# Kernel optimization log

Hardware: AMD Instinct MI355X
Metric: run time of the kernel (lower is better)

Reference implementation:

```python
import math
import jax, jax.numpy as jnp
import numpy as np

B, T, D, K, R, KC = 4, 2048, 1024, 8, 16, 4
H = 4 * D  # mlp hidden


def setup_inputs() -> dict:
    key = jax.random.key(0)
    ks = jax.random.split(key, 12)
    s = lambda i, shape: jax.random.normal(ks[i], shape, jnp.float32) * 0.02
    # state_decay_logit init: geometric decays in [dmin, dmax], logit = log(p) - log1p(-p)
    dmin, dmax = 0.9, 0.999
    dec = np.exp(np.linspace(math.log(dmin), math.log(dmax), K))
    decay_logit = jnp.asarray(np.log(dec) - np.log1p(-dec), jnp.float32)
    return dict(
        x=jax.random.normal(ks[0], (B, T, D), jnp.float32),
        conv_w=s(1, (D, 1, KC)),            # depthwise conv kernel (torch Conv1d weight)
        gp_w=s(2, (D, D)), gp_b=jnp.zeros((D,), jnp.float32),
        up_w=s(3, (D, H)), up_b=jnp.zeros((H,), jnp.float32),
        dn_w=s(4, (H, D)), dn_b=jnp.zeros((D,), jnp.float32),
        si_w=s(5, (D, K * D)),              # state_in (no bias)
        so_w=s(6, (K * D, D)),              # state_out (no bias)
        decay_logit=decay_logit,
        rs_w=s(7, (D, R)), rs_b=jnp.zeros((R,), jnp.float32),
        rwg_w=s(8, (D, 1)), rwg_b=jnp.zeros((1,), jnp.float32),
        rv_w=s(9, (D, D)), rv_b=jnp.zeros((D,), jnp.float32),
        gr_w=s(10, (D, 1)), gr_b=jnp.zeros((1,), jnp.float32),
        gl_w=s(11, (D, 1)), gl_b=jnp.zeros((1,), jnp.float32),
    )


def _rms_norm(x, eps=1e-6):
    return x * jax.lax.rsqrt(jnp.mean(x * x, axis=-1, keepdims=True) + eps)


def _forward(x, conv_w, gp_w, gp_b, up_w, up_b, dn_w, dn_b, si_w, so_w,
             decay_logit, rs_w, rs_b, rwg_w, rwg_b, rv_w, rv_b, gr_w, gr_b, gl_w, gl_b):
    Bx, Tx, Dx = x.shape
    u = _rms_norm(x)
    # --- local mixer: causal depthwise conv + sigmoid gate + SiLU MLP ---
    xc = jax.lax.conv_general_dilated(
        jnp.swapaxes(u, 1, 2), conv_w, window_strides=(1,),
        padding=[(KC - 1, 0)], feature_group_count=Dx,
        dimension_numbers=('NCH', 'OIH', 'NCH'))
    xc = jnp.swapaxes(xc, 1, 2)                       # (B,T,D) causal conv output
    xg = xc * jax.nn.sigmoid(xc @ gp_w + gp_b)
    local = jax.nn.silu(xg @ up_w + up_b) @ dn_w + dn_b
    # --- per-channel exponential-decay state + register read/write scan ---
    dec = jax.nn.sigmoid(decay_logit)                 # (K,)
    z = (u @ si_w).reshape(Bx, Tx, K, Dx)             # state_in, (B,T,K,D)
    sel = jax.nn.softmax(u @ rs_w + rs_b, axis=-1)    # soft register address (B,T,R)
    wg = jax.nn.sigmoid(u @ rwg_w + rwg_b)            # write gate (B,T,1)
    v = u @ rv_w + rv_b                                # register value (B,T,D)

    def step(carry, inp):
        s, regs = carry
        z_t, sel_t, w_t, v_t = inp
        read = jnp.einsum('br,brd->bd', sel_t, regs)  # soft read before write
        ws = (w_t * sel_t)[:, :, None]                # (B,R,1)
        regs = regs * (1.0 - ws) + ws * v_t[:, None, :]
        s = dec[None, :, None] * s + z_t
        return (s, regs), (s, read)

    init = (jnp.zeros((Bx, K, Dx), x.dtype), jnp.zeros((Bx, R, Dx), x.dtype))
    tm = lambda a: jnp.swapaxes(a, 0, 1)              # time-major for scan
    _, (s_all, reads) = jax.lax.scan(step, init, (tm(z), tm(sel), tm(wg), tm(v)))
    s_all = tm(s_all)                                 # (B,T,K,D)
    reads = tm(reads)                                 # (B,T,D)
    long_out = jnp.einsum('btkd,kde->bte', s_all, so_w.reshape(K, Dx, Dx))
    g_long = jax.nn.sigmoid(u @ gl_w + gl_b)
    g_reg = jax.nn.sigmoid(u @ gr_w + gr_b)
    return x + local + g_long * long_out + g_reg * reads


def reference(x, conv_w, gp_w, gp_b, up_w, up_b, dn_w, dn_b, si_w, so_w,
              decay_logit, rs_w, rs_b, rwg_w, rwg_b, rv_w, rv_b, gr_w, gr_b, gl_w, gl_b):
    return _forward(x, conv_w, gp_w, gp_b, up_w, up_b, dn_w, dn_b, si_w, so_w,
                    decay_logit, rs_w, rs_b, rwg_w, rwg_b, rv_w, rv_b, gr_w, gr_b, gl_w, gl_b)
```

## Files before the change

### kernel.cpp

```cpp
#include <hip/hip_runtime.h>

typedef unsigned short u16;
typedef __bf16 bf16x8 __attribute__((ext_vector_type(8)));
typedef float f32x4 __attribute__((ext_vector_type(4)));
typedef u16 u16x4 __attribute__((ext_vector_type(4)));

#define D_ 1024
#define T_ 2048
#define B_ 4
#define K_ 8
#define R_ 16
#define H_ 4096
#define NROW (B_*T_)
#define CH 32
#define CL (T_/CH)
#define CHS 64
#define CLS (T_/CHS)

__device__ __forceinline__ u16 f2bf(float f){
  union{float f;unsigned u;} v; v.f=f;
  unsigned r = v.u + 0x7FFFu + ((v.u>>16)&1u);
  return (u16)(r>>16);
}
__device__ __forceinline__ float bf2f(u16 b){
  union{unsigned u;float f;} v; v.u = ((unsigned)b)<<16; return v.f;
}
__device__ __forceinline__ float sigm(float x){ return 1.f/(1.f+__expf(-x)); }

__device__ __forceinline__ void gload_lds16(const void* g, void* l){
  __builtin_amdgcn_global_load_lds((const __attribute__((address_space(1))) void*)g,
                                   (__attribute__((address_space(3))) void*)l, 16, 0, 0);
}

__global__ __launch_bounds__(256) void fill_k(float* __restrict__ out, long n, float v){
  long i = (long)blockIdx.x*256 + threadIdx.x;
  if (i < n) out[i] = v;
}

__global__ __launch_bounds__(256) void transpose_cast(const float* __restrict__ in, u16* __restrict__ out,
                                                      int R, int C){
  __shared__ float tile[32][33];
  int bx = blockIdx.x*32;
  int by = blockIdx.y*32;
  int tx = threadIdx.x & 31, ty = threadIdx.x >> 5;
  #pragma unroll
  for (int i=0;i<32;i+=8) tile[ty+i][tx] = in[(size_t)(by+ty+i)*C + bx+tx];
  __syncthreads();
  #pragma unroll
  for (int i=0;i<32;i+=8) out[(size_t)(bx+ty+i)*R + by+tx] = f2bf(tile[tx][ty+i]);
}

__global__ __launch_bounds__(256) void castbf(const float* __restrict__ in, u16* __restrict__ out, long n){
  long i = (long)blockIdx.x*256 + threadIdx.x;
  if (i < n) out[i] = f2bf(in[i]);
}

__global__ __launch_bounds__(256) void initout_k(const float* __restrict__ x, const float* __restrict__ b,
                                                 float* __restrict__ out){
  size_t i = ((size_t)blockIdx.x*256 + threadIdx.x)*4;
  f32x4 xv = *(const f32x4*)(x + i);
  f32x4 bv = *(const f32x4*)(b + (i & (D_-1)));
  xv += bv;
  *(f32x4*)(out + i) = xv;
}

__global__ __launch_bounds__(256) void rmsnorm_k(const float* __restrict__ x, u16* __restrict__ u){
  int row = blockIdx.x;
  const float* xr = x + (size_t)row*D_;
  float xv[4]; float ss = 0.f;
  #pragma unroll
  for (int i=0;i<4;i++){ xv[i] = xr[threadIdx.x + 256*i]; ss += xv[i]*xv[i]; }
  #pragma unroll
  for (int o=32;o>0;o>>=1) ss += __shfl_down(ss, o);
  __shared__ float red[4];
  if ((threadIdx.x&63)==0) red[threadIdx.x>>6] = ss;
  __syncthreads();
  float tot = red[0]+red[1]+red[2]+red[3];
  float r = rsqrtf(tot*(1.f/D_) + 1e-6f);
  #pragma unroll
  for (int i=0;i<4;i++) u[(size_t)row*D_ + threadIdx.x + 256*i] = f2bf(xv[i]*r);
}

__global__ __launch_bounds__(256) void conv_k(const u16* __restrict__ u, const float* __restrict__ w,
                                              u16* __restrict__ xc){
  size_t base = ((size_t)blockIdx.x*256 + threadIdx.x)*4;
  int t  = (int)((base >> 10) & (T_-1));
  int d0 = (int)(base & (D_-1));
  f32x4 wv[4];
  #pragma unroll
  for (int jj=0;jj<4;jj++) wv[jj] = *(const f32x4*)&w[(d0+jj)*4];
  float acc[4] = {0.f,0.f,0.f,0.f};
  #pragma unroll
  for (int j=0;j<4;j++){
    if (t-3+j >= 0){
      u16x4 uv = *(const u16x4*)(u + base + (long)(j-3)*D_);
      #pragma unroll
      for (int jj=0;jj<4;jj++) acc[jj] += bf2f(uv[jj]) * wv[jj][j];
    }
  }
  u16x4 o;
  #pragma unroll
  for (int jj=0;jj<4;jj++) o[jj] = f2bf(acc[jj]);
  *(u16x4*)(xc + base) = o;
}

__global__ __launch_bounds__(256) void smalln_k(const u16* __restrict__ u,
    const float* __restrict__ rs_w, const float* __restrict__ rs_b,
    const float* __restrict__ rwg_w, const float* __restrict__ rwg_b,
    const float* __restrict__ gl_w, const float* __restrict__ gl_b,
    const float* __restrict__ gr_w, const float* __restrict__ gr_b,
    float* __restrict__ sel, float* __restrict__ wg, float* __restrict__ gl, float* __restrict__ gr){
  int row = blockIdx.x, tid = threadIdx.x;
  float p[19];
  #pragma unroll
  for (int c=0;c<19;c++) p[c] = 0.f;
  for (int i=0;i<4;i++){
    int e = tid + i*256;
    float ue = bf2f(u[(size_t)row*D_ + e]);
    const float* rw = rs_w + (size_t)e*16;
    #pragma unroll
    for (int r=0;r<16;r++) p[r] += ue*rw[r];
    p[16] += ue*rwg_w[e];
    p[17] += ue*gl_w[e];
    p[18] += ue*gr_w[e];
  }
  __shared__ float red[19*4];
  #pragma unroll
  for (int c=0;c<19;c++){
    float v = p[c];
    #pragma unroll
    for (int o=32;o>0;o>>=1) v += __shfl_down(v, o);
    if ((tid&63)==0) red[c*4 + (tid>>6)] = v;
  }
  __syncthreads();
  if (tid==0){
    float s[19];
    #pragma unroll
    for (int c=0;c<19;c++) s[c] = red[c*4]+red[c*4+1]+red[c*4+2]+red[c*4+3];
    float mx = -1e30f;
    #pragma unroll
    for (int r=0;r<16;r++){ s[r] += rs_b[r]; mx = fmaxf(mx, s[r]); }
    float ssum = 0.f;
    #pragma unroll
    for (int r=0;r<16;r++){ s[r] = __expf(s[r]-mx); ssum += s[r]; }
    float inv = 1.f/ssum;
    #pragma unroll
    for (int r=0;r<16;r++) sel[(size_t)row*16+r] = s[r]*inv;
    wg[row] = sigm(s[16] + rwg_b[0]);
    gl[row] = sigm(s[17] + gl_b[0]);
    gr[row] = sigm(s[18] + gr_b[0]);
  }
}

#define BM 128
#define BN 128
#define BK 32

template<int EPI>
__global__ __launch_bounds__(256)
void gemm_bt(const u16* __restrict__ A, const u16* __restrict__ BT,
             void* __restrict__ outp, const float* __restrict__ bias,
             const void* __restrict__ aux,
             int K, int lda, int ldb, int ldc,
             long zA, long zB, long zC)
{
  __shared__ __attribute__((aligned(16))) u16 As[BM*BK];
  __shared__ __attribute__((aligned(16))) u16 Bs[BN*BK];
  int nwg = gridDim.x*gridDim.y;
  int bx = blockIdx.x, by = blockIdx.y;
  if ((nwg & 7) == 0){
    int bid = blockIdx.y*gridDim.x + blockIdx.x;
    int cpx = nwg >> 3;
    int s = (bid & 7)*cpx + (bid >> 3);
    bx = s % gridDim.x; by = s / gridDim.x;
  }
  const u16* Ab = A + (size_t)blockIdx.z*zA + (size_t)bx*BM*lda;
  const u16* Bb = BT + (size_t)blockIdx.z*zB + (size_t)by*BN*ldb;
  int tid = threadIdx.x, lane = tid&63, wid = tid>>6;
  int wr = wid>>1, wc = wid&1;
  f32x4 acc[4][4];
  #pragma unroll
  for (int m=0;m<4;m++)
    #pragma unroll
    for (int n=0;n<4;n++) acc[m][n] = (f32x4){0.f,0.f,0.f,0.f};

  int srow = lane>>2;
  int scol = (lane&3)*8;
  int klo  = (lane>>4)*8;
  for (int k0=0; k0<K; k0+=BK){
    #pragma unroll
    for (int i=0;i<2;i++){
      int r0 = wid*32 + i*16;
      gload_lds16(Ab + (size_t)(r0+srow)*lda + k0 + scol, &As[r0*BK]);
      gload_lds16(Bb + (size_t)(r0+srow)*ldb + k0 + scol, &Bs[r0*BK]);
    }
    __syncthreads();
    bf16x8 af[4], bfr[4];
    #pragma unroll
    for (int m=0;m<4;m++) af[m] = *(const bf16x8*)&As[(wr*64+m*16+(lane&15))*BK + klo];
    #pragma unroll
    for (int n=0;n<4;n++) bfr[n] = *(const bf16x8*)&Bs[(wc*64+n*16+(lane&15))*BK + klo];
    #pragma unroll
    for (int m=0;m<4;m++)
      #pragma unroll
      for (int n=0;n<4;n++)
        acc[m][n] = __builtin_amdgcn_mfma_f32_16x16x32_bf16(af[m], bfr[n], acc[m][n], 0, 0, 0);
    __syncthreads();
  }

  size_t obase = (size_t)blockIdx.z*zC;
  int row0 = bx*BM + wr*64;
  int col0 = by*BN + wc*64;
  #pragma unroll
  for (int m=0;m<4;m++){
    #pragma unroll
    for (int n=0;n<4;n++){
      int col = col0 + n*16 + (lane&15);
      #pragma unroll
      for (int r=0;r<4;r++){
        int row = row0 + m*16 + (lane>>4)*4 + r;
        float c = acc[m][n][r];
        size_t idx = obase + (size_t)row*ldc + col;
        if (EPI==0){ ((u16*)outp)[idx] = f2bf(c); }
        else if (EPI==1){ ((u16*)outp)[idx] = f2bf(c + bias[col]); }
        else if (EPI==2){ float t=c+bias[col]; ((u16*)outp)[idx] = f2bf(bf2f(((const u16*)aux)[idx]) * sigm(t)); }
        else if (EPI==3){ float t=c+bias[col]; ((u16*)outp)[idx] = f2bf(t*sigm(t)); }
        else if (EPI==4){ ((float*)outp)[idx] = ((const float*)aux)[idx] + c + bias[col]; }
        else            { ((float*)outp)[idx] += c; }
      }
    }
  }
}

template<int NT, int EPI>
__global__ __launch_bounds__(512, 2)
void gemm8p(const u16* __restrict__ A, const u16* __restrict__ BT,
            void* __restrict__ outp, const float* __restrict__ bias,
            const void* __restrict__ aux,
            int lda, int ldb, int ldc, long zA, long zB, long zC,
            int rx, int ry, int nry)
{
  __shared__ __attribute__((aligned(16))) u16 lds8[65536];
  int bid = blockIdx.y*gridDim.x + blockIdx.x;
  int xcd = bid & 7;
  int s   = bid >> 3;
  int rgx = xcd / nry, rgy = xcd - rgx*nry;
  int bx = rgx*rx + (s % rx);
  int by = rgy*ry + (s / rx);

  const u16* Ab = A + (size_t)blockIdx.z*zA + (size_t)bx*256*lda;
  const u16* Bb = BT + (size_t)blockIdx.z*zB + (size_t)by*256*ldb;

  int tid = threadIdx.x, l = tid&63, w = tid>>6;
  int wr = w>>2, wc = w&3;
  int rS0 = (w*2+0)*8 + (l>>3);
  int rS1 = (w*2+1)*8 + (l>>3);
  int cg  = (((l&7) ^ (l>>3)) << 3);
  int seg0 = (w*2+0)*512;
  int seg1 = (w*2+1)*512;

  auto STAGE = [&](int h){
    int kt = h>>2, idx = h&3, par = kt&1;
    int koff = kt*64;
    if (idx < 2){
      const u16* s0 = Bb + (size_t)(idx*128 + rS0)*ldb + koff + cg;
      const u16* s1 = Bb + (size_t)(idx*128 + rS1)*ldb + koff + cg;
      u16* d = &lds8[par*32768 + 16384 + idx*8192];
      gload_lds16(s0, d + seg0);
      gload_lds16(s1, d + seg1);
    } else {
      int a = idx-2;
      const u16* s0 = Ab + (size_t)(a*128 + rS0)*lda + koff + cg;
      const u16* s1 = Ab + (size_t)(a*128 + rS1)*lda + koff + cg;
      u16* d = &lds8[par*32768 + a*8192];
      gload_lds16(s0, d + seg0);
      gload_lds16(s1, d + seg1);
    }
  };

  f32x4 acc[8][4];
  #pragma unroll
  for (int m=0;m<8;m++)
    #pragma unroll
    for (int n=0;n<4;n++) acc[m][n] = (f32x4){0.f,0.f,0.f,0.f};

  for (int h=0; h<7; ++h) STAGE(h);
  asm volatile("s_waitcnt vmcnt(6)" ::: "memory");
  __builtin_amdgcn_s_barrier();

  for (int it=0; it<NT/2; ++it){
    #pragma unroll
    for (int sub=0; sub<2; ++sub){
      int kt = it*2+sub;
      const int par = sub;
      u16* Abase = &lds8[par*32768 + wr*8192];
      u16* Bbase = &lds8[par*32768 + 16384 + (wc>>1)*8192];
      bf16x8 bf[4][2];
      #pragma unroll
      for (int q=0; q<4; ++q){
        bf16x8 af[2][2];
        if (q==0){
          #pragma unroll
          for (int n=0;n<4;n++)
            #pragma unroll
            for (int ss=0;ss<2;ss++){
              int rr = (wc&1)*64 + n*16 + (l&15);
              int c16 = (l>>4) + ss*4;
              bf[n][ss] = *(const bf16x8*)&Bbase[rr*64 + ((c16 ^ (rr&7))<<3)];
            }
        }
        #pragma unroll
        for (int i=0;i<2;i++)
          #pragma unroll
          for (int ss=0;ss<2;ss++){
            int rr = q*32 + i*16 + (l&15);
            int c16 = (l>>4) + ss*4;
            af[i][ss] = *(const bf16x8*)&Abase[rr*64 + ((c16 ^ (rr&7))<<3)];
          }
        __builtin_amdgcn_sched_barrier(0);
        int h = kt*4 + q + 7;
        if (h < 4*NT) STAGE(h);
        __builtin_amdgcn_s_barrier();
        asm volatile("s_waitcnt lgkmcnt(0)" ::: "memory");
        __builtin_amdgcn_sched_barrier(0);
        __builtin_amdgcn_s_setprio(1);
        #pragma unroll
        for (int i=0;i<2;i++)
          #pragma unroll
          for (int n=0;n<4;n++)
            #pragma unroll
            for (int ss=0;ss<2;ss++)
              acc[q*2+i][n] = __builtin_amdgcn_mfma_f32_16x16x32_bf16(af[i][ss], bf[n][ss], acc[q*2+i][n], 0, 0, 0);
        __builtin_amdgcn_s_setprio(0);
        if (q==3){
          if (kt == NT-2)      asm volatile("s_waitcnt vmcnt(0)" ::: "memory");
          else if (kt < NT-2)  asm volatile("s_waitcnt vmcnt(6)" ::: "memory");
        }
        __builtin_amdgcn_s_barrier();
      }
    }
  }

  size_t obase = (size_t)blockIdx.z*zC;
  int row0 = bx*256 + wr*128;
  int col0 = by*256 + wc*64;
  #pragma unroll
  for (int m=0;m<8;m++){
    #pragma unroll
    for (int n=0;n<4;n++){
      int col = col0 + n*16 + (l&15);
      #pragma unroll
      for (int r=0;r<4;r++){
        int row = row0 + m*16 + (l>>4)*4 + r;
        float c = acc[m][n][r];
        size_t idx = obase + (size_t)row*ldc + col;
        if (EPI==0){ ((u16*)outp)[idx] = f2bf(c); }
        else if (EPI==1){ ((u16*)outp)[idx] = f2bf(c + bias[col]); }
        else if (EPI==2){ float t=c+bias[col]; ((u16*)outp)[idx] = f2bf(bf2f(((const u16*)aux)[idx]) * sigm(t)); }
        else if (EPI==3){ float t=c+bias[col]; ((u16*)outp)[idx] = f2bf(t*sigm(t)); }
        else            { unsafeAtomicAdd(&((float*)outp)[idx], c); }
      }
    }
  }
}

template<int NT>
__global__ __launch_bounds__(512, 2)
void gemm8z(const u16* __restrict__ A, const u16* __restrict__ BT,
            void* __restrict__ outp, const float* __restrict__ bias,
            const float* __restrict__ bias2, const void* __restrict__ aux,
            int lda, int ldb, int ldc, long zA, long zB, long zC,
            int rx, int ry, int nry)
{
  __shared__ __attribute__((aligned(16))) u16 lds8[65536];
  int bid = blockIdx.y*gridDim.x + blockIdx.x;
  int xcd = bid & 7;
  int s   = bid >> 3;
  int rgx = xcd / nry, rgy = xcd - rgx*nry;
  int bx = rgx*rx + (s % rx);
  int by = rgy*ry + (s / rx);

  const u16* Ab = A + (size_t)blockIdx.z*zA + (size_t)bx*256*lda;
  const u16* Bb = BT + (size_t)blockIdx.z*zB + (size_t)by*256*ldb;

  int tid = threadIdx.x, l = tid&63, w = tid>>6;
  int wr = w>>2, wc = w&3;
  int rS0 = (w*2+0)*8 + (l>>3);
  int rS1 = (w*2+1)*8 + (l>>3);
  int cg  = (((l&7) ^ (l>>3)) << 3);
  int seg0 = (w*2+0)*512;
  int seg1 = (w*2+1)*512;

  auto STAGE = [&](int h){
    int kt = h>>2, idx = h&3, par = kt&1;
    int koff = kt*64;
    if (idx < 2){
      const u16* s0 = Bb + (size_t)(idx*128 + rS0)*ldb + koff + cg;
      const u16* s1 = Bb + (size_t)(idx*128 + rS1)*ldb + koff + cg;
      u16* d = &lds8[par*32768 + 16384 + idx*8192];
      gload_lds16(s0, d + seg0);
      gload_lds16(s1, d + seg1);
    } else {
      int a = idx-2;
      const u16* s0 = Ab + (size_t)(a*128 + rS0)*lda + koff + cg;
      const u16* s1 = Ab + (size_t)(a*128 + rS1)*lda + koff + cg;
      u16* d = &lds8[par*32768 + a*8192];
      gload_lds16(s0, d + seg0);
      gload_lds16(s1, d + seg1);
    }
  };

  f32x4 acc[8][4];
  #pragma unroll
  for (int m=0;m<8;m++)
    #pragma unroll
    for (int n=0;n<4;n++) acc[m][n] = (f32x4){0.f,0.f,0.f,0.f};

  for (int h=0; h<7; ++h) STAGE(h);
  asm volatile("s_waitcnt vmcnt(6)" ::: "memory");
  __builtin_amdgcn_s_barrier();

  for (int it=0; it<NT/2; ++it){
    #pragma unroll
    for (int sub=0; sub<2; ++sub){
      int kt = it*2+sub;
      const int par = sub;
      u16* Abase = &lds8[par*32768 + wr*8192];
      u16* Bbase = &lds8[par*32768 + 16384 + (wc>>1)*8192];
      bf16x8 bf[4][2];
      #pragma unroll
      for (int q=0; q<4; ++q){
        bf16x8 af[2][2];
        if (q==0){
          #pragma unroll
          for (int n=0;n<4;n++)
            #pragma unroll
            for (int ss=0;ss<2;ss++){
              int rr = (wc&1)*64 + n*16 + (l&15);
              int c16 = (l>>4) + ss*4;
              bf[n][ss] = *(const bf16x8*)&Bbase[rr*64 + ((c16 ^ (rr&7))<<3)];
            }
        }
        #pragma unroll
        for (int i=0;i<2;i++)
          #pragma unroll
          for (int ss=0;ss<2;ss++){
            int rr = q*32 + i*16 + (l&15);
            int c16 = (l>>4) + ss*4;
            af[i][ss] = *(const bf16x8*)&Abase[rr*64 + ((c16 ^ (rr&7))<<3)];
          }
        __builtin_amdgcn_sched_barrier(0);
        int h = kt*4 + q + 7;
        if (h < 4*NT) STAGE(h);
        __builtin_amdgcn_s_barrier();
        asm volatile("s_waitcnt lgkmcnt(0)" ::: "memory");
        __builtin_amdgcn_sched_barrier(0);
        __builtin_amdgcn_s_setprio(1);
        #pragma unroll
        for (int i=0;i<2;i++)
          #pragma unroll
          for (int n=0;n<4;n++)
            #pragma unroll
            for (int ss=0;ss<2;ss++)
              acc[q*2+i][n] = __builtin_amdgcn_mfma_f32_16x16x32_bf16(af[i][ss], bf[n][ss], acc[q*2+i][n], 0, 0, 0);
        __builtin_amdgcn_s_setprio(0);
        if (q==3){
          if (kt == NT-2)      asm volatile("s_waitcnt vmcnt(0)" ::: "memory");
          else if (kt < NT-2)  asm volatile("s_waitcnt vmcnt(6)" ::: "memory");
        }
        __builtin_amdgcn_s_barrier();
      }
    }
  }

  size_t obase = (size_t)blockIdx.z*zC;
  int row0 = bx*256 + wr*128;
  int col0 = by*256 + wc*64;
  bool z0 = (blockIdx.z == 0);
  #pragma unroll
  for (int m=0;m<8;m++){
    #pragma unroll
    for (int n=0;n<4;n++){
      int col = col0 + n*16 + (l&15);
      #pragma unroll
      for (int r=0;r<4;r++){
        int row = row0 + m*16 + (l>>4)*4 + r;
        float c = acc[m][n][r];
        size_t idx = obase + (size_t)row*ldc + col;
        if (z0){ float t=c+bias[col]; ((u16*)outp)[idx] = f2bf(bf2f(((const u16*)aux)[idx]) * sigm(t)); }
        else   { ((u16*)outp)[idx] = f2bf(c + bias2[col]); }
      }
    }
  }
}

template<int NT, int EPI>
__global__ __launch_bounds__(512, 2)
void gemm2p(const u16* __restrict__ A, const u16* __restrict__ BT,
            void* __restrict__ outp, const float* __restrict__ bias,
            const void* __restrict__ aux,
            int lda, int ldb, int ldc, long zA, long zB, long zC,
            int rx, int ry, int nry)
{
  __shared__ __attribute__((aligned(16))) u16 lds8[65536];
  int bid = blockIdx.y*gridDim.x + blockIdx.x;
  int xcd = bid & 7;
  int s   = bid >> 3;
  int rgx = xcd / nry, rgy = xcd - rgx*nry;
  int bx = rgx*rx + (s % rx);
  int by = rgy*ry + (s / rx);

  const u16* Ab = A + (size_t)blockIdx.z*zA + (size_t)bx*256*lda;
  const u16* Bb = BT + (size_t)blockIdx.z*zB + (size_t)by*256*ldb;

  int tid = threadIdx.x, l = tid&63, w = tid>>6;
  int wr = w>>2, wc = w&3;
  int cg  = (((l&7) ^ (l>>3)) << 3);
  const u16* gA0 = Ab + (size_t)((w*2+0)*8 + (l>>3))*lda + cg;
  const u16* gA1 = Ab + (size_t)((w*2+1)*8 + (l>>3))*lda + cg;
  const u16* gB0 = Bb + (size_t)((w*2+0)*8 + (l>>3))*ldb + cg;
  const u16* gB1 = Bb + (size_t)((w*2+1)*8 + (l>>3))*ldb + cg;
  size_t a128 = (size_t)128*lda, b128 = (size_t)128*ldb;
  int seg0 = (w*2+0)*512, seg1 = (w*2+1)*512;

  auto STAGE_TILE = [&](int par){
    u16* Ad = &lds8[par*32768];
    u16* Bd = &lds8[par*32768 + 16384];
    gload_lds16(gB0,        Bd + seg0);
    gload_lds16(gB1,        Bd + seg1);
    gload_lds16(gB0 + b128, Bd + 8192 + seg0);
    gload_lds16(gB1 + b128, Bd + 8192 + seg1);
    gload_lds16(gA0,        Ad + seg0);
    gload_lds16(gA1,        Ad + seg1);
    gload_lds16(gA0 + a128, Ad + 8192 + seg0);
    gload_lds16(gA1 + a128, Ad + 8192 + seg1);
    gA0 += 64; gA1 += 64; gB0 += 64; gB1 += 64;
  };

  f32x4 acc[8][4];
  #pragma unroll
  for (int m=0;m<8;m++)
    #pragma unroll
    for (int n=0;n<4;n++) acc[m][n] = (f32x4){0.f,0.f,0.f,0.f};

  STAGE_TILE(0);
  asm volatile("s_waitcnt vmcnt(0)" ::: "memory");
  __builtin_amdgcn_s_barrier();
  __builtin_amdgcn_sched_barrier(0);

  for (int kt=0; kt<NT; ++kt){
    int par = kt&1;
    if (kt+1 < NT) STAGE_TILE(par^1);
    u16* Abase = &lds8[par*32768 + wr*8192];
    u16* Bbase = &lds8[par*32768 + 16384 + (wc>>1)*8192];
    bf16x8 bf[4][2];
    #pragma unroll
    for (int n=0;n<4;n++)
      #pragma unroll
      for (int ss=0;ss<2;ss++){
        int rr = (wc&1)*64 + n*16 + (l&15);
        int c16 = (l>>4) + ss*4;
        bf[n][ss] = *(const bf16x8*)&Bbase[rr*64 + ((c16 ^ (rr&7))<<3)];
      }
    __builtin_amdgcn_s_setprio(1);
    #pragma unroll
    for (int q=0;q<4;q++){
      bf16x8 af[2][2];
      #pragma unroll
      for (int i=0;i<2;i++)
        #pragma unroll
        for (int ss=0;ss<2;ss++){
          int rr = q*32 + i*16 + (l&15);
          int c16 = (l>>4) + ss*4;
          af[i][ss] = *(const bf16x8*)&Abase[rr*64 + ((c16 ^ (rr&7))<<3)];
        }
      #pragma unroll
      for (int i=0;i<2;i++)
        #pragma unroll
        for (int n=0;n<4;n++)
          #pragma unroll
          for (int ss=0;ss<2;ss++)
            acc[q*2+i][n] = __builtin_amdgcn_mfma_f32_16x16x32_bf16(af[i][ss], bf[n][ss], acc[q*2+i][n], 0, 0, 0);
    }
    __builtin_amdgcn_s_setprio(0);
    asm volatile("s_waitcnt vmcnt(0)" ::: "memory");
    __builtin_amdgcn_s_barrier();
    __builtin_amdgcn_sched_barrier(0);
  }

  size_t obase = (size_t)blockIdx.z*zC;
  int row0 = bx*256 + wr*128;
  int col0 = by*256 + wc*64;
  #pragma unroll
  for (int m=0;m<8;m++){
    #pragma unroll
    for (int n=0;n<4;n++){
      int col = col0 + n*16 + (l&15);
      #pragma unroll
      for (int r=0;r<4;r++){
        int row = row0 + m*16 + (l>>4)*4 + r;
        float c = acc[m][n][r];
        size_t idx = obase + (size_t)row*ldc + col;
        if (EPI==0){ ((u16*)outp)[idx] = f2bf(c); }
        else if (EPI==1){ ((u16*)outp)[idx] = f2bf(c + bias[col]); }
        else if (EPI==2){ float t=c+bias[col]; ((u16*)outp)[idx] = f2bf(bf2f(((const u16*)aux)[idx]) * sigm(t)); }
        else if (EPI==3){ float t=c+bias[col]; ((u16*)outp)[idx] = f2bf(t*sigm(t)); }
        else            { unsafeAtomicAdd(&((float*)outp)[idx], c); }
      }
    }
  }
}

template<int KH>
__global__ __launch_bounds__(256) void scan_s1v(const u16* __restrict__ y, const float* __restrict__ logit,
                                                int p, float* __restrict__ Hend){
  int e0 = threadIdx.x*4;
  int c = blockIdx.y, b = blockIdx.z;
  float dec[KH]; f32x4 h[KH];
  #pragma unroll
  for (int k=0;k<KH;k++){ dec[k] = sigm(logit[KH*p+k]); h[k] = (f32x4){0.f,0.f,0.f,0.f}; }
  size_t row0 = (size_t)b*T_ + (size_t)c*CLS;
  for (int t=0;t<CLS;t++){
    const u16* yp = y + (row0+t)*(size_t)(KH*D_) + e0;
    #pragma unroll
    for (int k=0;k<KH;k++){
      u16x4 w = *(const u16x4*)(yp + (size_t)k*D_);
      #pragma unroll
      for (int j=0;j<4;j++) h[k][j] = dec[k]*h[k][j] + bf2f(w[j]);
    }
  }
  #pragma unroll
  for (int k=0;k<KH;k++)
    *(f32x4*)&Hend[(((size_t)b*CHS+c)*KH+k)*D_ + e0] = h[k];
}

template<int KH>
__global__ __launch_bounds__(256) void scan_s2v(const float* __restrict__ Hend, const float* __restrict__ logit,
                                                int p, float* __restrict__ Sinit){
  int idx = blockIdx.x*256 + threadIdx.x;
  if (idx >= B_*KH*D_) return;
  int e = idx % D_; int kh = (idx/D_) % KH; int b = idx/(D_*KH);
  float dec = sigm(logit[KH*p+kh]);
  float dL = powf(dec, (float)CLS);
  float carry = 0.f;
  for (int c=0;c<CHS;c++){
    size_t i3 = (((size_t)b*CHS+c)*KH+kh)*D_ + e;
    Sinit[i3] = carry;
    carry = dL*carry + Hend[i3];
  }
}

template<int KH>
__global__ __launch_bounds__(256) void scan_s3v(const u16* __restrict__ y, const float* __restrict__ logit,
                                                int p, const float* __restrict__ Sinit,
                                                const float* __restrict__ glb, float* __restrict__ out){
  int e0 = threadIdx.x*4;
  int c = blockIdx.y, b = blockIdx.z;
  float dec[KH]; f32x4 h[KH];
  #pragma unroll
  for (int k=0;k<KH;k++){
    dec[k] = sigm(logit[KH*p+k]);
    h[k] = *(const f32x4*)&Sinit[(((size_t)b*CHS+c)*KH+k)*D_ + e0];
  }
  size_t row0 = (size_t)b*T_ + (size_t)c*CLS;
  for (int t=0;t<CLS;t++){
    const u16* yp = y + (row0+t)*(size_t)(KH*D_) + e0;
    f32x4 sum = (f32x4){0.f,0.f,0.f,0.f};
    #pragma unroll
    for (int k=0;k<KH;k++){
      u16x4 w = *(const u16x4*)(yp + (size_t)k*D_);
      #pragma unroll
      for (int j=0;j<4;j++){ h[k][j] = dec[k]*h[k][j] + bf2f(w[j]); sum[j] += h[k][j]; }
    }
    float g = glb[row0+t];
    f32x4* op = (f32x4*)&out[(row0+t)*D_ + e0];
    f32x4 ov = *op;
    #pragma unroll
    for (int j=0;j<4;j++) ov[j] += g*sum[j];
    *op = ov;
  }
}

__global__ __launch_bounds__(256) void scan_r1(const u16* __restrict__ v, const float* __restrict__ sel,
                                               const float* __restrict__ wg,
                                               float* __restrict__ Rend, float* __restrict__ Pout){
  int d = blockIdx.x*256 + threadIdx.x;
  int c = blockIdx.y, b = blockIdx.z;
  __shared__ float sel_s[CL*R_];
  __shared__ float wg_s[CL];
  size_t row0 = (size_t)b*T_ + (size_t)c*CL;
  for (int i=threadIdx.x; i<CL*R_; i+=256) sel_s[i] = sel[row0*R_ + i];
  for (int i=threadIdx.x; i<CL;    i+=256) wg_s[i]  = wg[row0 + i];
  __syncthreads();
  float regs[R_], P[R_];
  #pragma unroll
  for (int r=0;r<R_;r++){ regs[r]=0.f; P[r]=1.f; }
  for (int t=0;t<CL;t++){
    float vv = bf2f(v[(row0+t)*D_ + d]);
    float w = wg_s[t];
    #pragma unroll
    for (int r=0;r<R_;r++){
      float ws = w*sel_s[t*R_+r];
      regs[r] += ws*(vv - regs[r]);
      P[r] *= (1.f - ws);
    }
  }
  #pragma unroll
  for (int r=0;r<R_;r++) Rend[(((size_t)b*CH+c)*R_+r)*D_ + d] = regs[r];
  if (blockIdx.x==0 && threadIdx.x==0){
    #pragma unroll
    for (int r=0;r<R_;r++) Pout[((size_t)b*CH+c)*R_ + r] = P[r];
  }
}

__global__ __launch_bounds__(256) void scan_r2(const float* __restrict__ Rend, const float* __restrict__ Pbuf,
                                               float* __restrict__ Rinit){
  int idx = blockIdx.x*256 + threadIdx.x;
  if (idx >= B_*D_) return;
  int d = idx % D_; int b = idx / D_;
  float regs[R_];
  #pragma unroll
  for (int r=0;r<R_;r++) regs[r] = 0.f;
  for (int c=0;c<CH;c++){
    #pragma unroll
    for (int r=0;r<R_;r++){
      size_t i3 = (((size_t)b*CH+c)*R_+r)*D_ + d;
      Rinit[i3] = regs[r];
      regs[r] = Pbuf[((size_t)b*CH+c)*R_+r]*regs[r] + Rend[i3];
    }
  }
}

__global__ __launch_bounds__(256) void scan_r3(const u16* __restrict__ v, const float* __restrict__ sel,
                                               const float* __restrict__ wg, const float* __restrict__ Rinit,
                                               const float* __restrict__ grb, float* __restrict__ out){
  int d = blockIdx.x*256 + threadIdx.x;
  int c = blockIdx.y, b = blockIdx.z;
  __shared__ float sel_s[CL*R_];
  __shared__ float wg_s[CL];
  size_t row0 = (size_t)b*T_ + (size_t)c*CL;
  for (int i=threadIdx.x; i<CL*R_; i+=256) sel_s[i] = sel[row0*R_ + i];
  for (int i=threadIdx.x; i<CL;    i+=256) wg_s[i]  = wg[row0 + i];
  __syncthreads();
  float regs[R_];
  #pragma unroll
  for (int r=0;r<R_;r++) regs[r] = Rinit[(((size_t)b*CH+c)*R_+r)*D_ + d];
  for (int t=0;t<CL;t++){
    float vv = bf2f(v[(row0+t)*D_ + d]);
    float w = wg_s[t];
    float read = 0.f;
    #pragma unroll
    for (int r=0;r<R_;r++){
      float sr = sel_s[t*R_+r];
      read += sr*regs[r];
      float ws = w*sr;
      regs[r] += ws*(vv - regs[r]);
    }
    out[(row0+t)*D_ + d] += grb[row0+t]*read;
  }
}

static void launch_gemm(int epi, dim3 g, const u16* A, const u16* BT, void* out,
                        const float* bias, const void* aux, int K, int lda, int ldb, int ldc,
                        long zA, long zB, long zC, hipStream_t s){
  switch(epi){
    case 0: gemm_bt<0><<<g,256,0,s>>>(A,BT,out,bias,aux,K,lda,ldb,ldc,zA,zB,zC); break;
    case 1: gemm_bt<1><<<g,256,0,s>>>(A,BT,out,bias,aux,K,lda,ldb,ldc,zA,zB,zC); break;
    case 2: gemm_bt<2><<<g,256,0,s>>>(A,BT,out,bias,aux,K,lda,ldb,ldc,zA,zB,zC); break;
    case 3: gemm_bt<3><<<g,256,0,s>>>(A,BT,out,bias,aux,K,lda,ldb,ldc,zA,zB,zC); break;
    case 4: gemm_bt<4><<<g,256,0,s>>>(A,BT,out,bias,aux,K,lda,ldb,ldc,zA,zB,zC); break;
    default: gemm_bt<5><<<g,256,0,s>>>(A,BT,out,bias,aux,K,lda,ldb,ldc,zA,zB,zC); break;
  }
}

extern "C" void kernel_launch(void* const* d_in, const int* in_sizes, int n_in,
                              void* d_out, int out_size, void* d_ws, size_t ws_size,
                              hipStream_t stream){
  const float* x      = (const float*)d_in[0];
  const float* conv_w = (const float*)d_in[1];
  const float* gp_w   = (const float*)d_in[2];
  const float* gp_b   = (const float*)d_in[3];
  const float* up_w   = (const float*)d_in[4];
  const float* up_b   = (const float*)d_in[5];
  const float* dn_w   = (const float*)d_in[6];
  const float* dn_b   = (const float*)d_in[7];
  const float* si_w   = (const float*)d_in[8];
  const float* so_w   = (const float*)d_in[9];
  const float* logit  = (const float*)d_in[10];
  const float* rs_w   = (const float*)d_in[11];
  const float* rs_b   = (const float*)d_in[12];
  const float* rwg_w  = (const float*)d_in[13];
  const float* rwg_b  = (const float*)d_in[14];
  const float* rv_w   = (const float*)d_in[15];
  const float* rv_b   = (const float*)d_in[16];
  const float* gr_w   = (const float*)d_in[17];
  const float* gr_b   = (const float*)d_in[18];
  const float* gl_w   = (const float*)d_in[19];
  const float* gl_b   = (const float*)d_in[20];
  float* out = (float*)d_out;
  char* base = (char*)d_ws;

  {
    size_t off = 0;
    auto al = [&](size_t b)->char*{ char* r = base+off; off += (b+255)&~(size_t)255; return r; };
    char* u_r    = al((size_t)NROW*D_*2);
    char* v_r    = al((size_t)NROW*D_*2);
    char* big    = al((size_t)121634816);
    float* sel   = (float*)al((size_t)NROW*R_*4);
    float* wgb   = (float*)al((size_t)NROW*4);
    float* glb   = (float*)al((size_t)NROW*4);
    float* grb   = (float*)al((size_t)NROW*4);
    float* Pbuf  = (float*)al((size_t)B_*CH*R_*4);
    float* Rend  = (float*)al((size_t)B_*CH*R_*D_*4);
    float* Rinit = (float*)al((size_t)B_*CH*R_*D_*4);
    if (off <= ws_size){
      u16* u_bf  = (u16*)u_r;
      u16* v_bf  = (u16*)v_r;
      u16* hid   = (u16*)big;
      u16* xc_bf = (u16*)(big + (size_t)67108864);
      u16* xg_bf = (u16*)(big + (size_t)83886080);
      u16* gpT   = (u16*)(big + (size_t)100663296);
      u16* upT   = (u16*)(big + (size_t)102760448);
      u16* dnT   = (u16*)(big + (size_t)111149056);
      u16* rvT   = (u16*)(big + (size_t)119537664);
      u16* WT    = (u16*)big;
      u16* si_bf = (u16*)(big + (size_t)16777216);
      u16* soT   = (u16*)(big + (size_t)33554432);
      u16* y_bf  = (u16*)(big + (size_t)16777216);
      float* Hend  = (float*)(big + (size_t)83886080);
      float* Sinit = (float*)(big + (size_t)88080384);

      transpose_cast<<<dim3(D_/32, D_/32),256,0,stream>>>(gp_w, gpT, D_, D_);
      transpose_cast<<<dim3(H_/32, D_/32),256,0,stream>>>(up_w, upT, D_, H_);
      transpose_cast<<<dim3(D_/32, H_/32),256,0,stream>>>(dn_w, dnT, H_, D_);
      transpose_cast<<<dim3(D_/32, D_/32),256,0,stream>>>(rv_w, rvT, D_, D_);

      rmsnorm_k<<<NROW,256,0,stream>>>(x, u_bf);
      conv_k<<<(NROW*D_)/1024,256,0,stream>>>(u_bf, conv_w, xc_bf);
      smalln_k<<<NROW,256,0,stream>>>(u_bf, rs_w, rs_b, rwg_w, rwg_b, gl_w, gl_b, gr_w, gr_b,
                                      sel, wgb, glb, grb);

      gemm8z<16><<<dim3(NROW/256, D_/256, 2), 512, 0, stream>>>(
          xc_bf, gpT, xg_bf, gp_b, rv_b, xc_bf, D_, D_, D_,
          (long)(u_bf - xc_bf), (long)(rvT - gpT), (long)(v_bf - xg_bf), 4, 4, 1);

      gemm2p<16,3><<<dim3(NROW/256, H_/256), 512, 0, stream>>>(
          xg_bf, upT, hid, up_b, nullptr, D_, D_, H_, 0, 0, 0, 8, 8, 2);

      initout_k<<<(NROW*D_)/1024,256,0,stream>>>(x, dn_b, out);
      gemm8p<32,5><<<dim3(NROW/256, D_/256, 2), 512, 0, stream>>>(
          hid, dnT, out, nullptr, nullptr, H_, H_, D_, 2048, 2048, 0, 4, 4, 1);

      transpose_cast<<<dim3(D_/32, (K_*D_)/32),256,0,stream>>>(so_w, soT, K_*D_, D_);
      castbf<<<((long)D_*K_*D_+255)/256,256,0,stream>>>(si_w, si_bf, (long)D_*K_*D_);
      gemm8p<16,0><<<dim3(D_/256, D_/256, K_), 512, 0, stream>>>(
          soT, si_bf, WT, nullptr, nullptr, K_*D_, K_*D_, D_, (long)D_, (long)D_, (long)D_*D_, 2, 1, 4);

      for (int h=0; h<2; h++){
        gemm8p<16,0><<<dim3(NROW/256, (4*D_)/256), 512, 0, stream>>>(
            u_bf, WT + (size_t)h*4*D_*D_, y_bf, nullptr, nullptr, D_, D_, 4*D_, 0, 0, 0, 8, 8, 2);
        scan_s1v<4><<<dim3(1, CHS, B_),256,0,stream>>>(y_bf, logit, h, Hend);
        scan_s2v<4><<<(B_*4*D_+255)/256,256,0,stream>>>(Hend, logit, h, Sinit);
        scan_s3v<4><<<dim3(1, CHS, B_),256,0,stream>>>(y_bf, logit, h, Sinit, glb, out);
      }

      scan_r1<<<dim3(D_/256, CH, B_),256,0,stream>>>(v_bf, sel, wgb, Rend, Pbuf);
      scan_r2<<<(B_*D_+255)/256,256,0,stream>>>(Rend, Pbuf, Rinit);
      scan_r3<<<dim3(D_/256, CH, B_),256,0,stream>>>(v_bf, sel, wgb, Rinit, grb, out);
      return;
    }
  }

  const size_t MB16_8 = (size_t)NROW*D_*2;
  size_t off = 0;
  auto alloc = [&](size_t bytes)->char*{
    char* r = base + off; off += (bytes + 255) & ~(size_t)255; return r;
  };
  char* R0 = alloc(MB16_8);
  char* R1 = alloc(MB16_8);
  char* R2 = alloc(2*MB16_8);
  char* R3 = alloc((size_t)21*1024*1024);
  float* sel  = (float*)alloc((size_t)NROW*R_*4);
  float* wgb  = (float*)alloc((size_t)NROW*4);
  float* glb  = (float*)alloc((size_t)NROW*4);
  float* grb  = (float*)alloc((size_t)NROW*4);
  float* Pbuf = (float*)alloc((size_t)B_*CH*R_*4);
  float* Hend = (float*)alloc((size_t)B_*CHS*2*D_*4);
  float* Sinit= (float*)alloc((size_t)B_*CHS*2*D_*4);
  if (off > ws_size){
    fill_k<<<((long)out_size+255)/256,256,0,stream>>>(out, out_size, 12345.0f);
    return;
  }

  u16* u_bf  = (u16*)R0;
  u16* v_bf  = (u16*)R1;
  u16* xc_bf = (u16*)R2;
  u16* xg_bf = (u16*)(R2 + MB16_8);
  u16* hid_bf= (u16*)R2;
  u16* soT   = (u16*)R2;
  u16* si_bf = (u16*)(R2 + MB16_8);
  u16* y_bf  = (u16*)R2;
  u16* gpT   = (u16*)R3;
  u16* upT   = (u16*)(R3 + (size_t)2*1024*1024 + 131072);
  u16* dnT   = (u16*)(R3 + (size_t)10*1024*1024 + 655360);
  u16* rvT   = (u16*)(R3 + (size_t)19*1024*1024);
  u16* WT    = (u16*)R3;
  float* Rend = (float*)R3;
  float* Rinit= (float*)(R3 + (size_t)NROW*D_);

  transpose_cast<<<dim3(D_/32, D_/32),256,0,stream>>>(gp_w, gpT, D_, D_);
  transpose_cast<<<dim3(H_/32, D_/32),256,0,stream>>>(up_w, upT, D_, H_);
  transpose_cast<<<dim3(D_/32, H_/32),256,0,stream>>>(dn_w, dnT, H_, D_);
  transpose_cast<<<dim3(D_/32, D_/32),256,0,stream>>>(rv_w, rvT, D_, D_);

  rmsnorm_k<<<NROW,256,0,stream>>>(x, u_bf);
  conv_k<<<(NROW*D_)/1024,256,0,stream>>>(u_bf, conv_w, xc_bf);
  smalln_k<<<NROW,256,0,stream>>>(u_bf, rs_w, rs_b, rwg_w, rwg_b, gl_w, gl_b, gr_w, gr_b,
                                  sel, wgb, glb, grb);

  launch_gemm(2, dim3(NROW/BM, D_/BN, 1), xc_bf, gpT, xg_bf, gp_b, xc_bf,
              D_, D_, D_, D_, 0, 0, 0, stream);
  launch_gemm(1, dim3(NROW/BM, D_/BN, 1), u_bf, rvT, v_bf, rv_b, nullptr,
              D_, D_, D_, D_, 0, 0, 0, stream);
  for (int q=0; q<4; q++){
    launch_gemm(3, dim3(NROW/BM, 1024/BN, 1), xg_bf, upT + (size_t)q*1024*D_, hid_bf,
                up_b + q*1024, nullptr, D_, D_, D_, 1024, 0, 0, 0, stream);
    launch_gemm(q==0?4:5, dim3(NROW/BM, D_/BN, 1), hid_bf, dnT + (size_t)q*1024, out,
                dn_b, x, 1024, 1024, H_, D_, 0, 0, 0, stream);
  }

  transpose_cast<<<dim3(D_/32, (K_*D_)/32),256,0,stream>>>(so_w, soT, K_*D_, D_);
  castbf<<<((long)D_*K_*D_+255)/256,256,0,stream>>>(si_w, si_bf, (long)D_*K_*D_);
  launch_gemm(0, dim3(D_/BM, D_/BN, K_), soT, si_bf, WT, nullptr, nullptr,
              D_, K_*D_, K_*D_, D_, (long)D_, (long)D_, (long)D_*D_, stream);

  for (int p=0; p<4; p++){
    launch_gemm(0, dim3(NROW/BM, (2*D_)/BN, 1), u_bf, WT + (size_t)(2*p)*D_*D_, y_bf,
                nullptr, nullptr, D_, D_, D_, 2*D_, 0, 0, 0, stream);
    scan_s1v<2><<<dim3(1, CHS, B_),256,0,stream>>>(y_bf, logit, p, Hend);
    scan_s2v<2><<<(B_*2*D_+255)/256,256,0,stream>>>(Hend, logit, p, Sinit);
    scan_s3v<2><<<dim3(1, CHS, B_),256,0,stream>>>(y_bf, logit, p, Sinit, glb, out);
  }

  scan_r1<<<dim3(D_/256, CH, B_),256,0,stream>>>(v_bf, sel, wgb, Rend, Pbuf);
  scan_r2<<<(B_*D_+255)/256,256,0,stream>>>(Rend, Pbuf, Rinit);
  scan_r3<<<dim3(D_/256, CH, B_),256,0,stream>>>(v_bf, sel, wgb, Rinit, grb, out);
}
```

Baseline: 707.8 us.

## Add finer-grained pipelined GEMM variant and parallelize decay scan over heads

```diff
diff --git a/kernel.cpp b/kernel.cpp
--- a/kernel.cpp
+++ b/kernel.cpp
@@ -496,7 +496,7 @@
 
 template<int NT, int EPI>
 __global__ __launch_bounds__(512, 2)
-void gemm2p(const u16* __restrict__ A, const u16* __restrict__ BT,
+void gemm4p(const u16* __restrict__ A, const u16* __restrict__ BT,
             void* __restrict__ outp, const float* __restrict__ bias,
             const void* __restrict__ aux,
             int lda, int ldb, int ldc, long zA, long zB, long zC,
@@ -515,26 +515,30 @@
 
   int tid = threadIdx.x, l = tid&63, w = tid>>6;
   int wr = w>>2, wc = w&3;
+  int rS0 = (w*2+0)*8 + (l>>3);
+  int rS1 = (w*2+1)*8 + (l>>3);
   int cg  = (((l&7) ^ (l>>3)) << 3);
-  const u16* gA0 = Ab + (size_t)((w*2+0)*8 + (l>>3))*lda + cg;
-  const u16* gA1 = Ab + (size_t)((w*2+1)*8 + (l>>3))*lda + cg;
-  const u16* gB0 = Bb + (size_t)((w*2+0)*8 + (l>>3))*ldb + cg;
-  const u16* gB1 = Bb + (size_t)((w*2+1)*8 + (l>>3))*ldb + cg;
-  size_t a128 = (size_t)128*lda, b128 = (size_t)128*ldb;
-  int seg0 = (w*2+0)*512, seg1 = (w*2+1)*512;
-
-  auto STAGE_TILE = [&](int par){
-    u16* Ad = &lds8[par*32768];
-    u16* Bd = &lds8[par*32768 + 16384];
-    gload_lds16(gB0,        Bd + seg0);
-    gload_lds16(gB1,        Bd + seg1);
-    gload_lds16(gB0 + b128, Bd + 8192 + seg0);
-    gload_lds16(gB1 + b128, Bd + 8192 + seg1);
-    gload_lds16(gA0,        Ad + seg0);
-    gload_lds16(gA1,        Ad + seg1);
-    gload_lds16(gA0 + a128, Ad + 8192 + seg0);
-    gload_lds16(gA1 + a128, Ad + 8192 + seg1);
-    gA0 += 64; gA1 += 64; gB0 += 64; gB1 += 64;
+  int seg0 = (w*2+0)*512;
+  int seg1 = (w*2+1)*512;
+
+  auto STAGE = [&](int h){
+    if (h >= 4*NT) return;
+    int kt = h>>2, idx = h&3, par = kt&1;
+    int koff = kt*64;
+    if (idx < 2){
+      const u16* s0 = Bb + (size_t)(idx*128 + rS0)*ldb + koff + cg;
+      const u16* s1 = Bb + (size_t)(idx*128 + rS1)*ldb + koff + cg;
+      u16* d = &lds8[par*32768 + 16384 + idx*8192];
+      gload_lds16(s0, d + seg0);
+      gload_lds16(s1, d + seg1);
+    } else {
+      int a = idx-2;
+      const u16* s0 = Ab + (size_t)(a*128 + rS0)*lda + koff + cg;
+      const u16* s1 = Ab + (size_t)(a*128 + rS1)*lda + koff + cg;
+      u16* d = &lds8[par*32768 + a*8192];
+      gload_lds16(s0, d + seg0);
+      gload_lds16(s1, d + seg1);
+    }
   };
 
   f32x4 acc[8][4];
@@ -543,14 +547,12 @@
     #pragma unroll
     for (int n=0;n<4;n++) acc[m][n] = (f32x4){0.f,0.f,0.f,0.f};
 
-  STAGE_TILE(0);
-  asm volatile("s_waitcnt vmcnt(0)" ::: "memory");
+  for (int h=0; h<7; ++h) STAGE(h);
+  asm volatile("s_waitcnt vmcnt(6)" ::: "memory");
   __builtin_amdgcn_s_barrier();
-  __builtin_amdgcn_sched_barrier(0);
 
   for (int kt=0; kt<NT; ++kt){
-    int par = kt&1;
-    if (kt+1 < NT) STAGE_TILE(par^1);
+    const int par = kt&1;
     u16* Abase = &lds8[par*32768 + wr*8192];
     u16* Bbase = &lds8[par*32768 + 16384 + (wc>>1)*8192];
     bf16x8 bf[4][2];
@@ -562,30 +564,64 @@
         int c16 = (l>>4) + ss*4;
         bf[n][ss] = *(const bf16x8*)&Bbase[rr*64 + ((c16 ^ (rr&7))<<3)];
       }
-    __builtin_amdgcn_s_setprio(1);
-    #pragma unroll
-    for (int q=0;q<4;q++){
-      bf16x8 af[2][2];
+    bf16x8 afA[2][2][2];
+    #pragma unroll
+    for (int qq=0;qq<2;qq++)
       #pragma unroll
       for (int i=0;i<2;i++)
         #pragma unroll
         for (int ss=0;ss<2;ss++){
-          int rr = q*32 + i*16 + (l&15);
+          int rr = qq*32 + i*16 + (l&15);
           int c16 = (l>>4) + ss*4;
-          af[i][ss] = *(const bf16x8*)&Abase[rr*64 + ((c16 ^ (rr&7))<<3)];
+          afA[qq][i][ss] = *(const bf16x8*)&Abase[rr*64 + ((c16 ^ (rr&7))<<3)];
         }
+    STAGE(kt*4 + 7);
+    STAGE(kt*4 + 8);
+    __builtin_amdgcn_s_barrier();
+    asm volatile("s_waitcnt lgkmcnt(0)" ::: "memory");
+    __builtin_amdgcn_sched_barrier(0);
+    __builtin_amdgcn_s_setprio(1);
+    #pragma unroll
+    for (int qq=0;qq<2;qq++)
       #pragma unroll
       for (int i=0;i<2;i++)
         #pragma unroll
         for (int n=0;n<4;n++)
           #pragma unroll
           for (int ss=0;ss<2;ss++)
-            acc[q*2+i][n] = __builtin_amdgcn_mfma_f32_16x16x32_bf16(af[i][ss], bf[n][ss], acc[q*2+i][n], 0, 0, 0);
-    }
+            acc[qq*2+i][n] = __builtin_amdgcn_mfma_f32_16x16x32_bf16(afA[qq][i][ss], bf[n][ss], acc[qq*2+i][n], 0, 0, 0);
     __builtin_amdgcn_s_setprio(0);
-    asm volatile("s_waitcnt vmcnt(0)" ::: "memory");
     __builtin_amdgcn_s_barrier();
+    bf16x8 afB[2][2][2];
+    #pragma unroll
+    for (int qq=0;qq<2;qq++)
+      #pragma unroll
+      for (int i=0;i<2;i++)
+        #pragma unroll
+        for (int ss=0;ss<2;ss++){
+          int rr = (qq+2)*32 + i*16 + (l&15);
+          int c16 = (l>>4) + ss*4;
+          afB[qq][i][ss] = *(const bf16x8*)&Abase[rr*64 + ((c16 ^ (rr&7))<<3)];
+        }
+    STAGE(kt*4 + 9);
+    STAGE(kt*4 + 10);
+    __builtin_amdgcn_s_barrier();
+    asm volatile("s_waitcnt lgkmcnt(0)" ::: "memory");
     __builtin_amdgcn_sched_barrier(0);
+    __builtin_amdgcn_s_setprio(1);
+    #pragma unroll
+    for (int qq=0;qq<2;qq++)
+      #pragma unroll
+      for (int i=0;i<2;i++)
+        #pragma unroll
+        for (int n=0;n<4;n++)
+          #pragma unroll
+          for (int ss=0;ss<2;ss++)
+            acc[(qq+2)*2+i][n] = __builtin_amdgcn_mfma_f32_16x16x32_bf16(afB[qq][i][ss], bf[n][ss], acc[(qq+2)*2+i][n], 0, 0, 0);
+    __builtin_amdgcn_s_setprio(0);
+    if (kt == NT-2)      asm volatile("s_waitcnt vmcnt(0)" ::: "memory");
+    else if (kt < NT-2)  asm volatile("s_waitcnt vmcnt(6)" ::: "memory");
+    __builtin_amdgcn_s_barrier();
   }
 
   size_t obase = (size_t)blockIdx.z*zC;
@@ -603,7 +639,6 @@
         size_t idx = obase + (size_t)row*ldc + col;
         if (EPI==0){ ((u16*)outp)[idx] = f2bf(c); }
         else if (EPI==1){ ((u16*)outp)[idx] = f2bf(c + bias[col]); }
-        else if (EPI==2){ float t=c+bias[col]; ((u16*)outp)[idx] = f2bf(bf2f(((const u16*)aux)[idx]) * sigm(t)); }
         else if (EPI==3){ float t=c+bias[col]; ((u16*)outp)[idx] = f2bf(t*sigm(t)); }
         else            { unsafeAtomicAdd(&((float*)outp)[idx], c); }
       }
@@ -612,26 +647,20 @@
 }
 
 template<int KH>
-__global__ __launch_bounds__(256) void scan_s1v(const u16* __restrict__ y, const float* __restrict__ logit,
+__global__ __launch_bounds__(256) void scan_s1k(const u16* __restrict__ y, const float* __restrict__ logit,
                                                 int p, float* __restrict__ Hend){
+  int k = blockIdx.x;
   int e0 = threadIdx.x*4;
   int c = blockIdx.y, b = blockIdx.z;
-  float dec[KH]; f32x4 h[KH];
-  #pragma unroll
-  for (int k=0;k<KH;k++){ dec[k] = sigm(logit[KH*p+k]); h[k] = (f32x4){0.f,0.f,0.f,0.f}; }
+  float dec = sigm(logit[KH*p+k]);
+  f32x4 h = (f32x4){0.f,0.f,0.f,0.f};
   size_t row0 = (size_t)b*T_ + (size_t)c*CLS;
   for (int t=0;t<CLS;t++){
-    const u16* yp = y + (row0+t)*(size_t)(KH*D_) + e0;
-    #pragma unroll
-    for (int k=0;k<KH;k++){
-      u16x4 w = *(const u16x4*)(yp + (size_t)k*D_);
-      #pragma unroll
-      for (int j=0;j<4;j++) h[k][j] = dec[k]*h[k][j] + bf2f(w[j]);
-    }
-  }
-  #pragma unroll
-  for (int k=0;k<KH;k++)
-    *(f32x4*)&Hend[(((size_t)b*CHS+c)*KH+k)*D_ + e0] = h[k];
+    u16x4 w = *(const u16x4*)(y + (row0+t)*(size_t)(KH*D_) + (size_t)k*D_ + e0);
+    #pragma unroll
+    for (int j=0;j<4;j++) h[j] = dec*h[j] + bf2f(w[j]);
+  }
+  *(f32x4*)&Hend[(((size_t)b*CHS+c)*KH+k)*D_ + e0] = h;
 }
 
 template<int KH>
@@ -651,10 +680,10 @@
 }
 
 template<int KH>
-__global__ __launch_bounds__(256) void scan_s3v(const u16* __restrict__ y, const float* __restrict__ logit,
+__global__ __launch_bounds__(128) void scan_s3v(const u16* __restrict__ y, const float* __restrict__ logit,
                                                 int p, const float* __restrict__ Sinit,
                                                 const float* __restrict__ glb, float* __restrict__ out){
-  int e0 = threadIdx.x*4;
+  int e0 = (blockIdx.x*128 + threadIdx.x)*4;
   int c = blockIdx.y, b = blockIdx.z;
   float dec[KH]; f32x4 h[KH];
   #pragma unroll
@@ -844,7 +873,7 @@
           xc_bf, gpT, xg_bf, gp_b, rv_b, xc_bf, D_, D_, D_,
           (long)(u_bf - xc_bf), (long)(rvT - gpT), (long)(v_bf - xg_bf), 4, 4, 1);
 
-      gemm2p<16,3><<<dim3(NROW/256, H_/256), 512, 0, stream>>>(
+      gemm8p<16,3><<<dim3(NROW/256, H_/256), 512, 0, stream>>>(
           xg_bf, upT, hid, up_b, nullptr, D_, D_, H_, 0, 0, 0, 8, 8, 2);
 
       initout_k<<<(NROW*D_)/1024,256,0,stream>>>(x, dn_b, out);
@@ -856,12 +885,21 @@
       gemm8p<16,0><<<dim3(D_/256, D_/256, K_), 512, 0, stream>>>(
           soT, si_bf, WT, nullptr, nullptr, K_*D_, K_*D_, D_, (long)D_, (long)D_, (long)D_*D_, 2, 1, 4);
 
-      for (int h=0; h<2; h++){
+      {
+        int h = 0;
+        gemm4p<16,0><<<dim3(NROW/256, (4*D_)/256), 512, 0, stream>>>(
+            u_bf, WT + (size_t)h*4*D_*D_, y_bf, nullptr, nullptr, D_, D_, 4*D_, 0, 0, 0, 8, 8, 2);
+        scan_s1k<4><<<dim3(4, CHS, B_),256,0,stream>>>(y_bf, logit, h, Hend);
+        scan_s2v<4><<<(B_*4*D_+255)/256,256,0,stream>>>(Hend, logit, h, Sinit);
+        scan_s3v<4><<<dim3(2, CHS, B_),128,0,stream>>>(y_bf, logit, h, Sinit, glb, out);
+      }
+      {
+        int h = 1;
         gemm8p<16,0><<<dim3(NROW/256, (4*D_)/256), 512, 0, stream>>>(
             u_bf, WT + (size_t)h*4*D_*D_, y_bf, nullptr, nullptr, D_, D_, 4*D_, 0, 0, 0, 8, 8, 2);
-        scan_s1v<4><<<dim3(1, CHS, B_),256,0,stream>>>(y_bf, logit, h, Hend);
+        scan_s1k<4><<<dim3(4, CHS, B_),256,0,stream>>>(y_bf, logit, h, Hend);
         scan_s2v<4><<<(B_*4*D_+255)/256,256,0,stream>>>(Hend, logit, h, Sinit);
-        scan_s3v<4><<<dim3(1, CHS, B_),256,0,stream>>>(y_bf, logit, h, Sinit, glb, out);
+        scan_s3v<4><<<dim3(2, CHS, B_),128,0,stream>>>(y_bf, logit, h, Sinit, glb, out);
       }
 
       scan_r1<<<dim3(D_/256, CH, B_),256,0,stream>>>(v_bf, sel, wgb, Rend, Pbuf);
@@ -937,9 +975,9 @@
   for (int p=0; p<4; p++){
     launch_gemm(0, dim3(NROW/BM, (2*D_)/BN, 1), u_bf, WT + (size_t)(2*p)*D_*D_, y_bf,
                 nullptr, nullptr, D_, D_, D_, 2*D_, 0, 0, 0, stream);
-    scan_s1v<2><<<dim3(1, CHS, B_),256,0,stream>>>(y_bf, logit, p, Hend);
+    scan_s1k<2><<<dim3(2, CHS, B_),256,0,stream>>>(y_bf, logit, p, Hend);
     scan_s2v<2><<<(B_*2*D_+255)/256,256,0,stream>>>(Hend, logit, p, Sinit);
-    scan_s3v<2><<<dim3(1, CHS, B_),256,0,stream>>>(y_bf, logit, p, Sinit, glb, out);
+    scan_s3v<2><<<dim3(2, CHS, B_),128,0,stream>>>(y_bf, logit, p, Sinit, glb, out);
   }
 
   scan_r1<<<dim3(D_/256, CH, B_),256,0,stream>>>(v_bf, sel, wgb, Rend, Pbuf);
```

Measured after the change: 712.9 us. About the same (+0.7%).
